# Performance work log

Measured on AMD Instinct MI355X. Metric: run time of the kernel, lower is better.

## Reference

```python
import jax, jax.numpy as jnp
import numpy as np

MAX_SHIFT = 1  # kernel width = 2*MAX_SHIFT + 1 = 3


def setup_inputs() -> dict:
    key = jax.random.key(0)
    ks = jax.random.split(key, 7)
    B, N, M = 256, 4096, 64
    return {
        "memory": jax.random.normal(ks[0], (B, N, M), dtype=jnp.float32),
        "k": jax.random.normal(ks[1], (B, M), dtype=jnp.float32),
        "beta": jax.random.uniform(ks[2], (B, 1), dtype=jnp.float32),
        "prev_w": jax.random.uniform(ks[3], (B, N), dtype=jnp.float32),
        "g": jax.random.uniform(ks[4], (B, 1), dtype=jnp.float32),
        "s": jax.random.uniform(ks[5], (B, 2 * MAX_SHIFT + 1), dtype=jnp.float32),
        "gamma": jax.random.uniform(ks[6], (B, 1), dtype=jnp.float32),
    }


def reference(memory, k, beta, prev_w, g, s, gamma):
    eps = 1e-8
    # content addressing: cosine similarity of k against each memory row
    dot = jnp.einsum("bm,bnm->bn", k, memory)                      # [B,N]
    k_norm = jnp.maximum(jnp.linalg.norm(k, axis=1, keepdims=True), eps)   # [B,1]
    m_norm = jnp.maximum(jnp.linalg.norm(memory, axis=2), eps)             # [B,N]
    sim = dot / (k_norm * m_norm)
    w_c = jax.nn.softmax(beta * sim, axis=1)                       # [B,N]
    # gated interpolation
    w_g = g * w_c + (1.0 - g) * prev_w                             # [B,N]
    # circular shift: per-row correlation with kernel s (equivalent to the
    # original BxB conv1d + diagonal extraction)
    S = MAX_SHIFT
    N = w_g.shape[1]
    unrolled = jnp.concatenate([w_g[:, -S:], w_g, w_g[:, :S]], axis=1)  # [B,N+2S]
    windows = jnp.stack([unrolled[:, i:i + N] for i in range(2 * S + 1)], axis=1)  # [B,2S+1,N]
    w_s = jnp.einsum("bi,bin->bn", s, windows)                     # [B,N]
    # sharpen + normalize
    w_pow = w_s ** gamma
    return w_pow / (jnp.sum(w_pow, axis=1, keepdims=True) + 1e-16)
```

## Files before the change

### kernel.cpp

```cpp
#include <hip/hip_runtime.h>
#include <math.h>

#define NN 4096
#define MM 64
#define THREADS 1024

template <int CTRL>
__device__ __forceinline__ float dpp_add(float v) {
    int r = __builtin_amdgcn_update_dpp(0, __float_as_int(v), CTRL, 0xf, 0xf, true);
    return v + __int_as_float(r);
}

__device__ __forceinline__ float wave_red_sum(float v) {
#pragma unroll
    for (int o = 32; o > 0; o >>= 1) v += __shfl_down(v, o, 64);
    return v;
}
__device__ __forceinline__ float wave_red_max(float v) {
#pragma unroll
    for (int o = 32; o > 0; o >>= 1) v = fmaxf(v, __shfl_down(v, o, 64));
    return v;
}

__device__ __forceinline__ float block_sum(float v, float* scratch) {
    const int tid = threadIdx.x;
    const int lane = tid & 63, wid = tid >> 6;
    v = wave_red_sum(v);
    if (lane == 0) scratch[wid] = v;
    __syncthreads();
    if (tid < 64) {
        float x = (tid < 16) ? scratch[tid] : 0.0f;
        x = wave_red_sum(x);
        if (tid == 0) scratch[16] = x;
    }
    __syncthreads();
    float r = scratch[16];
    __syncthreads();
    return r;
}
__device__ __forceinline__ float block_max(float v, float* scratch) {
    const int tid = threadIdx.x;
    const int lane = tid & 63, wid = tid >> 6;
    v = wave_red_max(v);
    if (lane == 0) scratch[wid] = v;
    __syncthreads();
    if (tid < 64) {
        float x = (tid < 16) ? scratch[tid] : -INFINITY;
        x = wave_red_max(x);
        if (tid == 0) scratch[16] = x;
    }
    __syncthreads();
    float r = scratch[16];
    __syncthreads();
    return r;
}

extern "C" __global__ void __launch_bounds__(THREADS)
ntm_head_kernel(const float* __restrict__ memory, const float* __restrict__ k,
                const float* __restrict__ beta, const float* __restrict__ prev_w,
                const float* __restrict__ g, const float* __restrict__ s,
                const float* __restrict__ gamma, float* __restrict__ out) {
    __shared__ float dotA[NN];
    __shared__ float sqA[NN];
    __shared__ float wg[NN];
    __shared__ __align__(16) float kk[MM];
    __shared__ float scratch[32];
    __shared__ float knorm_sh;

    const int b = blockIdx.x;
    const int tid = threadIdx.x;
    const float* __restrict__ memB = memory + (size_t)b * NN * MM;

    float pw[4];
#pragma unroll
    for (int j = 0; j < 4; ++j)
        pw[j] = prev_w[(size_t)b * NN + tid + j * THREADS];
    const float beta_b = beta[b];
    const float g_b = g[b];
    const float s0 = s[b * 3], s1 = s[b * 3 + 1], s2 = s[b * 3 + 2];
    const float gamma_b = gamma[b];

    if (tid < 64) {
        const float kv = k[b * MM + tid];
        kk[tid] = kv;
        const float sk = wave_red_sum(kv * kv);
        if (tid == 0) knorm_sh = fmaxf(sqrtf(sk), 1e-8f);
    }
    __syncthreads();

    const int m4 = (tid & 15) * 4;
    const float kx = kk[m4], ky = kk[m4 + 1], kz = kk[m4 + 2], kw = kk[m4 + 3];

#pragma unroll 4
    for (int it = 0; it < 64; ++it) {
        const float4 mv = *(const float4*)(memB + (size_t)it * 4096 + tid * 4);
        float d = mv.x * kx + mv.y * ky + mv.z * kz + mv.w * kw;
        float q = mv.x * mv.x + mv.y * mv.y + mv.z * mv.z + mv.w * mv.w;
        d = dpp_add<0x111>(d);
        d = dpp_add<0x112>(d);
        d = dpp_add<0x114>(d);
        d = dpp_add<0x118>(d);
        q = dpp_add<0x111>(q);
        q = dpp_add<0x112>(q);
        q = dpp_add<0x114>(q);
        q = dpp_add<0x118>(q);
        if ((tid & 15) == 15) {
            const int n = it * 64 + (tid >> 4);
            dotA[n] = d;
            sqA[n] = q;
        }
    }
    __syncthreads();

    const float knorm = knorm_sh;

    float val[4];
    float lmax = -INFINITY;
#pragma unroll
    for (int j = 0; j < 4; ++j) {
        const int n = tid + j * THREADS;
        const float mn = fmaxf(sqrtf(sqA[n]), 1e-8f);
        const float v = beta_b * (dotA[n] / (knorm * mn));
        val[j] = v;
        lmax = fmaxf(lmax, v);
    }
    const float mx = block_max(lmax, scratch);

    float e[4];
    float lsum = 0.0f;
#pragma unroll
    for (int j = 0; j < 4; ++j) {
        e[j] = expf(val[j] - mx);
        lsum += e[j];
    }
    const float sumE = block_sum(lsum, scratch);

#pragma unroll
    for (int j = 0; j < 4; ++j) {
        const int n = tid + j * THREADS;
        const float wc = e[j] / sumE;
        wg[n] = g_b * wc + (1.0f - g_b) * pw[j];
    }
    __syncthreads();

    float wp[4];
    float lsum2 = 0.0f;
#pragma unroll
    for (int j = 0; j < 4; ++j) {
        const int n = tid + j * THREADS;
        const int nm = (n + NN - 1) & (NN - 1);
        const int np_ = (n + 1) & (NN - 1);
        const float ws = s0 * wg[nm] + s1 * wg[n] + s2 * wg[np_];
        const float p = (float)pow((double)ws, (double)gamma_b);
        wp[j] = p;
        lsum2 += p;
    }
    const float sumP = block_sum(lsum2, scratch);
    const float denom = sumP + 1e-16f;
#pragma unroll
    for (int j = 0; j < 4; ++j) {
        const int n = tid + j * THREADS;
        out[(size_t)b * NN + n] = wp[j] / denom;
    }
}

extern "C" void kernel_launch(void* const* d_in, const int* in_sizes, int n_in,
                              void* d_out, int out_size, void* d_ws, size_t ws_size,
                              hipStream_t stream) {
    const float* memory = (const float*)d_in[0];
    const float* k      = (const float*)d_in[1];
    const float* beta   = (const float*)d_in[2];
    const float* prev_w = (const float*)d_in[3];
    const float* g      = (const float*)d_in[4];
    const float* s      = (const float*)d_in[5];
    const float* gamma  = (const float*)d_in[6];
    float* out = (float*)d_out;

    const int B = in_sizes[2];
    ntm_head_kernel<<<B, THREADS, 0, stream>>>(memory, k, beta, prev_w, g, s, gamma, out);
}
```

Before: 379.0 us.

## Split NTM head into chunked memory-reduction kernel and per-batch softmax kernel

The single fused kernel, one 1024-thread block per batch row, is split in two. The first kernel uses 8 smaller blocks per batch row to stream the 268MB memory tensor and compute per-row dot products and squared norms, with a per-block phase offset to stagger addresses. It writes those pairs to a global workspace. A second kernel then does softmax, interpolation, shift and sharpen from that workspace. The aim is more blocks in flight and better occupancy for the bandwidth-bound pass, at the cost of an extra launch and a small global round-trip.

```diff
diff --git a/kernel.cpp b/kernel.cpp
--- a/kernel.cpp
+++ b/kernel.cpp
@@ -3,7 +3,10 @@
 
 #define NN 4096
 #define MM 64
-#define THREADS 1024
+#define K1_THREADS 256
+#define K1_CHUNKS 8
+#define ROWS_PER_CHUNK (NN / K1_CHUNKS)
+#define K2_THREADS 1024
 
 template <int CTRL>
 __device__ __forceinline__ float dpp_add(float v) {
@@ -55,46 +58,25 @@
     return r;
 }
 
-extern "C" __global__ void __launch_bounds__(THREADS)
-ntm_head_kernel(const float* __restrict__ memory, const float* __restrict__ k,
-                const float* __restrict__ beta, const float* __restrict__ prev_w,
-                const float* __restrict__ g, const float* __restrict__ s,
-                const float* __restrict__ gamma, float* __restrict__ out) {
-    __shared__ float dotA[NN];
-    __shared__ float sqA[NN];
-    __shared__ float wg[NN];
-    __shared__ __align__(16) float kk[MM];
-    __shared__ float scratch[32];
-    __shared__ float knorm_sh;
-
-    const int b = blockIdx.x;
+extern "C" __global__ void __launch_bounds__(K1_THREADS)
+ntm_phase_a(const float* __restrict__ memory, const float* __restrict__ k,
+            float2* __restrict__ ws2) {
     const int tid = threadIdx.x;
-    const float* __restrict__ memB = memory + (size_t)b * NN * MM;
-
-    float pw[4];
-#pragma unroll
-    for (int j = 0; j < 4; ++j)
-        pw[j] = prev_w[(size_t)b * NN + tid + j * THREADS];
-    const float beta_b = beta[b];
-    const float g_b = g[b];
-    const float s0 = s[b * 3], s1 = s[b * 3 + 1], s2 = s[b * 3 + 2];
-    const float gamma_b = gamma[b];
-
-    if (tid < 64) {
-        const float kv = k[b * MM + tid];
-        kk[tid] = kv;
-        const float sk = wave_red_sum(kv * kv);
-        if (tid == 0) knorm_sh = fmaxf(sqrtf(sk), 1e-8f);
-    }
-    __syncthreads();
+    const int b = blockIdx.x >> 3;
+    const int c = blockIdx.x & (K1_CHUNKS - 1);
+    const float* __restrict__ base =
+        memory + (size_t)b * NN * MM + (size_t)c * ROWS_PER_CHUNK * MM;
 
     const int m4 = (tid & 15) * 4;
-    const float kx = kk[m4], ky = kk[m4 + 1], kz = kk[m4 + 2], kw = kk[m4 + 3];
+    const float4 kf = *(const float4*)(k + b * MM + m4);
+
+    const int phase = (blockIdx.x * 5) & 31;
 
 #pragma unroll 4
-    for (int it = 0; it < 64; ++it) {
-        const float4 mv = *(const float4*)(memB + (size_t)it * 4096 + tid * 4);
-        float d = mv.x * kx + mv.y * ky + mv.z * kz + mv.w * kw;
+    for (int t = 0; t < 32; ++t) {
+        const int it = (t + phase) & 31;
+        const float4 mv = *(const float4*)(base + (size_t)it * 1024 + tid * 4);
+        float d = mv.x * kf.x + mv.y * kf.y + mv.z * kf.z + mv.w * kf.w;
         float q = mv.x * mv.x + mv.y * mv.y + mv.z * mv.z + mv.w * mv.w;
         d = dpp_add<0x111>(d);
         d = dpp_add<0x112>(d);
@@ -105,22 +87,49 @@
         q = dpp_add<0x114>(q);
         q = dpp_add<0x118>(q);
         if ((tid & 15) == 15) {
-            const int n = it * 64 + (tid >> 4);
-            dotA[n] = d;
-            sqA[n] = q;
+            const int n = c * ROWS_PER_CHUNK + it * 16 + (tid >> 4);
+            ws2[(size_t)b * NN + n] = make_float2(d, q);
         }
     }
+}
+
+extern "C" __global__ void __launch_bounds__(K2_THREADS)
+ntm_phase_b(const float2* __restrict__ ws2, const float* __restrict__ k,
+            const float* __restrict__ beta, const float* __restrict__ prev_w,
+            const float* __restrict__ g, const float* __restrict__ s,
+            const float* __restrict__ gamma, float* __restrict__ out) {
+    __shared__ float wg[NN];
+    __shared__ float scratch[32];
+    __shared__ float knorm_sh;
+
+    const int b = blockIdx.x;
+    const int tid = threadIdx.x;
+
+    float pw[4];
+#pragma unroll
+    for (int j = 0; j < 4; ++j)
+        pw[j] = prev_w[(size_t)b * NN + tid + j * K2_THREADS];
+    const float beta_b = beta[b];
+    const float g_b = g[b];
+    const float s0 = s[b * 3], s1 = s[b * 3 + 1], s2 = s[b * 3 + 2];
+    const float gamma_b = gamma[b];
+
+    if (tid < 64) {
+        const float kv = k[b * MM + tid];
+        const float sk = wave_red_sum(kv * kv);
+        if (tid == 0) knorm_sh = fmaxf(sqrtf(sk), 1e-8f);
+    }
     __syncthreads();
-
     const float knorm = knorm_sh;
 
     float val[4];
     float lmax = -INFINITY;
 #pragma unroll
     for (int j = 0; j < 4; ++j) {
-        const int n = tid + j * THREADS;
-        const float mn = fmaxf(sqrtf(sqA[n]), 1e-8f);
-        const float v = beta_b * (dotA[n] / (knorm * mn));
+        const int n = tid + j * K2_THREADS;
+        const float2 dq = ws2[(size_t)b * NN + n];
+        const float mn = fmaxf(sqrtf(dq.y), 1e-8f);
+        const float v = beta_b * (dq.x / (knorm * mn));
         val[j] = v;
         lmax = fmaxf(lmax, v);
     }
@@ -137,7 +146,7 @@
 
 #pragma unroll
     for (int j = 0; j < 4; ++j) {
-        const int n = tid + j * THREADS;
+        const int n = tid + j * K2_THREADS;
         const float wc = e[j] / sumE;
         wg[n] = g_b * wc + (1.0f - g_b) * pw[j];
     }
@@ -147,7 +156,7 @@
     float lsum2 = 0.0f;
 #pragma unroll
     for (int j = 0; j < 4; ++j) {
-        const int n = tid + j * THREADS;
+        const int n = tid + j * K2_THREADS;
         const int nm = (n + NN - 1) & (NN - 1);
         const int np_ = (n + 1) & (NN - 1);
         const float ws = s0 * wg[nm] + s1 * wg[n] + s2 * wg[np_];
@@ -159,7 +168,7 @@
     const float denom = sumP + 1e-16f;
 #pragma unroll
     for (int j = 0; j < 4; ++j) {
-        const int n = tid + j * THREADS;
+        const int n = tid + j * K2_THREADS;
         out[(size_t)b * NN + n] = wp[j] / denom;
     }
 }
@@ -175,7 +184,9 @@
     const float* s      = (const float*)d_in[5];
     const float* gamma  = (const float*)d_in[6];
     float* out = (float*)d_out;
+    float2* ws2 = (float2*)d_ws;
 
     const int B = in_sizes[2];
-    ntm_head_kernel<<<B, THREADS, 0, stream>>>(memory, k, beta, prev_w, g, s, gamma, out);
+    ntm_phase_a<<<B * K1_CHUNKS, K1_THREADS, 0, stream>>>(memory, k, ws2);
+    ntm_phase_b<<<B, K2_THREADS, 0, stream>>>(ws2, k, beta, prev_w, g, s, gamma, out);
 }
```

Measured after the change: 383.2 us. Within noise of the previous version (+1.1%).
